# Optimization experiments

Measured on AMD Instinct MI355X. Metric: run time of the kernel, lower is better.

## Reference

```python
import jax, jax.numpy as jnp
import numpy as np

NUM_EMBEDDINGS = 512
EMBEDDING_DIM = 100
COMMITMENT_COST = 0.25


def setup_inputs() -> dict:
    key = jax.random.key(0)
    k1, k2 = jax.random.split(key)
    inputs = jax.random.normal(k1, (64, 64, 64, EMBEDDING_DIM), dtype=jnp.float32)
    # nn.Embedding weight init: uniform(-1/num_embeddings, 1/num_embeddings)
    lim = 1.0 / NUM_EMBEDDINGS
    embedding = jax.random.uniform(k2, (NUM_EMBEDDINGS, EMBEDDING_DIM),
                                   dtype=jnp.float32, minval=-lim, maxval=lim)
    return {"inputs": inputs, "embedding": embedding}


def reference(inputs, embedding):
    d = inputs.shape[-1]
    flat = inputs.reshape(-1, d)                                  # [N, d]
    # squared L2 distances to each codebook entry: [N, K]
    distances = (jnp.sum(flat ** 2, axis=1, keepdims=True)
                 + jnp.sum(embedding ** 2, axis=1)
                 - 2.0 * flat @ embedding.T)
    encoding_indices = jnp.argmin(distances, axis=1)              # [N]
    quantized = embedding[encoding_indices].reshape(inputs.shape)
    commitment_loss = COMMITMENT_COST * jnp.mean(
        (jax.lax.stop_gradient(quantized) - inputs) ** 2)
    quantization_loss = jnp.mean(
        (quantized - jax.lax.stop_gradient(inputs)) ** 2)
    # straight-through estimator
    quantized_st = inputs + jax.lax.stop_gradient(quantized - inputs)
    return quantized_st, quantization_loss, commitment_loss
```

## Files before the change

### kernel.cpp

```cpp
#include <hip/hip_runtime.h>
#include <hip/hip_bf16.h>
#include <cfloat>


#define N_ROWS (64 * 64 * 64)
#define D 100
#define KCODES 512
#define CB_OFF 4096
#define E2_OFF 16

typedef __attribute__((ext_vector_type(8))) short short8;
typedef __attribute__((ext_vector_type(4))) float f32x4;

__device__ __forceinline__ unsigned short f2bf(float f) {
    union { float f; unsigned u; } v; v.f = f;
    unsigned r = v.u + 0x7FFF + ((v.u >> 16) & 1);
    return (unsigned short)(r >> 16);
}
__device__ __forceinline__ unsigned pk2(float a, float b) {
    union { __hip_bfloat162 h; unsigned u; } c;
    c.h = __float22bfloat162_rn(make_float2(a, b));
    return c.u;
}
__device__ __forceinline__ short8 pack8(const float4& a, const float4& b) {
    union { unsigned u[4]; short8 v; } r;
    r.u[0] = pk2(a.x, a.y); r.u[1] = pk2(a.z, a.w);
    r.u[2] = pk2(b.x, b.y); r.u[3] = pk2(b.z, b.w);
    return r.v;
}
__device__ __forceinline__ unsigned f2u(float f) {
    union { float f; unsigned u; } v; v.f = f; return v.u;
}
__device__ __forceinline__ float u2f(unsigned u) {
    union { unsigned u; float f; } v; v.u = u; return v.f;
}

__global__ __launch_bounds__(64) void vq_init(const float* __restrict__ emb,
                                              float* __restrict__ ws) {
    const int code = blockIdx.x, l = threadIdx.x;
    const float* e = emb + code * D;
    if (code == 0 && l == 0) ws[0] = 0.0f;
    float a = e[l];
    float b = (l < D - 64) ? e[64 + l] : 0.0f;
    float p = fmaf(a, a, b * b);
#pragma unroll
    for (int off = 32; off; off >>= 1) p += __shfl_xor(p, off);
    if (l == 0) ws[E2_OFF + code] = p;

    if (l < 16) {
        const int s = l >> 2, q = l & 3;
        short8 v;
#pragma unroll
        for (int j = 0; j < 8; ++j) {
            int k = s * 32 + q * 8 + j;
            v[j] = (k < D) ? (short)f2bf(e[k]) : (short)0;
        }
        if (l == 12) v[4] = (short)f2bf(-0.5f * p);
        const int chunk = code >> 5, ci = code & 31;
        const int tt = ci >> 4, lr = ci & 15;
        unsigned short* cb = (unsigned short*)((char*)ws + CB_OFF);
        *(short8*)(cb + chunk * 4096 + ((s * 2 + tt) * 64 + q * 16 + lr) * 8) = v;
    }
}

__global__ __launch_bounds__(256, 2) void vq_main(const float* __restrict__ x,
                                                  const float* __restrict__ emb,
                                                  float* __restrict__ ws,
                                                  float* __restrict__ out) {
    __shared__ uint4  bbuf[2][1024];
    __shared__ int    widx[256];
    __shared__ float  wsum[4];

    const int tid = threadIdx.x, wave = tid >> 6, lane = tid & 63;
    const int quad = lane >> 4, lr = lane & 15;
    const int lrc = 15 - lr;
    const long brow = (long)blockIdx.x * 256;
    const long wrow = brow + wave * 64;

    float4 av[4][7];
#pragma unroll
    for (int m = 0; m < 4; ++m) {
        const float* xr = x + (wrow + m * 16 + lr) * D + quad * 8;
        av[m][0] = *(const float4*)(xr);
        av[m][1] = *(const float4*)(xr + 4);
        av[m][2] = *(const float4*)(xr + 32);
        av[m][3] = *(const float4*)(xr + 36);
        av[m][4] = *(const float4*)(xr + 64);
        av[m][5] = *(const float4*)(xr + 68);
        av[m][6] = *(const float4*)(x + (wrow + m * 16 + lr) * D + 96);
    }

    const uint4* __restrict__ cbg = (const uint4*)((const char*)ws + CB_OFF);
    uint4 st0 = cbg[wave * 128 + lane];
    uint4 st1 = cbg[wave * 128 + 64 + lane];
    uint4 st2 = cbg[512 + wave * 128 + lane];
    uint4 st3 = cbg[512 + wave * 128 + 64 + lane];

    short8 A[4][4];
    float  xnorm[4];
    const float4 one0 = make_float4(quad == 0 ? 1.f : 0.f, 0.f, 0.f, 0.f);
#pragma unroll
    for (int m = 0; m < 4; ++m) {
        float4 z = av[m][6];
        if (quad != 0) z = make_float4(0.f, 0.f, 0.f, 0.f);
        float nrm = 0.f;
#pragma unroll
        for (int i = 0; i < 6; ++i) {
            float4 f = av[m][i];
            nrm = fmaf(f.x, f.x, nrm); nrm = fmaf(f.y, f.y, nrm);
            nrm = fmaf(f.z, f.z, nrm); nrm = fmaf(f.w, f.w, nrm);
        }
        nrm = fmaf(z.x, z.x, nrm); nrm = fmaf(z.y, z.y, nrm);
        nrm = fmaf(z.z, z.z, nrm); nrm = fmaf(z.w, z.w, nrm);
        A[m][0] = pack8(av[m][0], av[m][1]);
        A[m][1] = pack8(av[m][2], av[m][3]);
        A[m][2] = pack8(av[m][4], av[m][5]);
        A[m][3] = pack8(z, one0);
        nrm += __shfl_xor(nrm, 16);
        nrm += __shfl_xor(nrm, 32);
        xnorm[m] = nrm;
    }

    bbuf[0][wave * 128 + lane]             = st0;
    bbuf[0][wave * 128 + 64 + lane]        = st1;
    bbuf[0][512 + wave * 128 + lane]       = st2;
    bbuf[0][512 + wave * 128 + 64 + lane]  = st3;
    __syncthreads();

    float runpk[4][4];
#pragma unroll
    for (int m = 0; m < 4; ++m)
#pragma unroll
        for (int r = 0; r < 4; ++r) runpk[m][r] = -FLT_MAX;

#pragma unroll 1
    for (int j = 0; j < 8; ++j) {
        const int p = j & 1;
        uint4 n0, n1, n2, n3;
        if (j < 7) {
            n0 = cbg[(j + 1) * 1024 + wave * 128 + lane];
            n1 = cbg[(j + 1) * 1024 + wave * 128 + 64 + lane];
            n2 = cbg[(j + 1) * 1024 + 512 + wave * 128 + lane];
            n3 = cbg[(j + 1) * 1024 + 512 + wave * 128 + 64 + lane];
        }

#pragma unroll
        for (int cc = 0; cc < 2; ++cc) {
            const int c = j * 2 + cc;
            const short8* __restrict__ bl = (const short8*)&bbuf[p][cc * 512];
            short8 B[2][4];
#pragma unroll
            for (int s = 0; s < 4; ++s) {
                B[0][s] = bl[(s * 2 + 0) * 64 + lane];
                B[1][s] = bl[(s * 2 + 1) * 64 + lane];
            }

            f32x4 acc[4][2];
#pragma unroll
            for (int m = 0; m < 4; ++m) {
                acc[m][0] = (f32x4){0.f, 0.f, 0.f, 0.f};
                acc[m][1] = (f32x4){0.f, 0.f, 0.f, 0.f};
            }
#pragma unroll
            for (int s = 0; s < 4; ++s)
#pragma unroll
                for (int m = 0; m < 4; ++m) {
                    acc[m][0] = __builtin_amdgcn_mfma_f32_16x16x32_bf16(A[m][s], B[0][s], acc[m][0], 0, 0, 0);
                    acc[m][1] = __builtin_amdgcn_mfma_f32_16x16x32_bf16(A[m][s], B[1][s], acc[m][1], 0, 0, 0);
                }

            const int ib0 = (31 - (c * 2 + 0)) * 16 + lrc;
            const int ib1 = (31 - (c * 2 + 1)) * 16 + lrc;
#pragma unroll
            for (int m = 0; m < 4; ++m)
#pragma unroll
                for (int r = 0; r < 4; ++r) {
                    float p0 = u2f((f2u(acc[m][0][r]) & ~511u) | (unsigned)ib0);
                    float p1 = u2f((f2u(acc[m][1][r]) & ~511u) | (unsigned)ib1);
                    runpk[m][r] = fmaxf(runpk[m][r], fmaxf(p0, p1));
                }
        }

        if (j < 7) {
            bbuf[p ^ 1][wave * 128 + lane]            = n0;
            bbuf[p ^ 1][wave * 128 + 64 + lane]       = n1;
            bbuf[p ^ 1][512 + wave * 128 + lane]      = n2;
            bbuf[p ^ 1][512 + wave * 128 + 64 + lane] = n3;
        }
        __syncthreads();
    }

    float lsum = 0.0f;
#pragma unroll
    for (int m = 0; m < 4; ++m)
#pragma unroll
        for (int r = 0; r < 4; ++r) {
            float s = runpk[m][r];
#pragma unroll
            for (int off = 8; off >= 1; off >>= 1)
                s = fmaxf(s, __shfl_xor(s, off));
            if (lr == quad * 4 + r) {
                unsigned u = f2u(s);
                int code = 511 - (int)(u & 511u);
                lsum += fmaf(-2.0f, s, xnorm[m]);
                widx[wave * 64 + m * 16 + quad * 4 + r] = code;
            }
        }
#pragma unroll
    for (int off = 32; off >= 1; off >>= 1) lsum += __shfl_xor(lsum, off);
    if (lane == 0) wsum[wave] = lsum;
    __syncthreads();
    if (tid == 0) atomicAdd(ws, wsum[0] + wsum[1] + wsum[2] + wsum[3]);

    const float4* __restrict__ ef = (const float4*)emb;
    float4* __restrict__ og = (float4*)(out + brow * D);
#pragma unroll
    for (int i = 0; i < 25; i += 5) {
        float4 q[5];
        int    gi[5];
#pragma unroll
        for (int u = 0; u < 5; ++u) {
            int g = (i + u) * 256 + tid;
            int row = g / 25;
            int c4  = g - row * 25;
            gi[u] = g;
            q[u]  = ef[(long)widx[row] * 25 + c4];
        }
#pragma unroll
        for (int u = 0; u < 5; ++u) og[gi[u]] = q[u];
    }
}

__global__ void vq_final(const float* __restrict__ ws, float* __restrict__ out) {
    float mse = ws[0] / (float)((long)N_ROWS * D);
    out[(long)N_ROWS * D]     = mse;
    out[(long)N_ROWS * D + 1] = 0.25f * mse;
}

extern "C" void kernel_launch(void* const* d_in, const int* in_sizes, int n_in,
                              void* d_out, int out_size, void* d_ws, size_t ws_size,
                              hipStream_t stream) {
    const float* x   = (const float*)d_in[0];
    const float* emb = (const float*)d_in[1];
    float* out = (float*)d_out;
    float* ws  = (float*)d_ws;

    vq_init<<<KCODES, 64, 0, stream>>>(emb, ws);
    vq_main<<<N_ROWS / 256, 256, 0, stream>>>(x, emb, ws, out);
    vq_final<<<1, 1, 0, stream>>>(ws, out);
}
```

Measured before the change: 214.6 us.

## Switch distance GEMM from bf16 to fp8 MFMA with scaled codebook

Converts the input rows and codebook to fp8 e4m3 and uses the 16x16x32 fp8 MFMA instead of bf16. The codebook is pre-scaled by 512 so its tiny values fit the fp8 range, and the norm term is folded in with matching scaling. This halves codebook staging traffic and LDS footprint and raises MFMA throughput. The cost is much coarser distances, which risks wrong argmin choices and loss values that no longer match the reference.

Result: no change. 213.4 us (-0.5%).

```diff
diff --git a/kernel.cpp b/kernel.cpp
--- a/kernel.cpp
+++ b/kernel.cpp
@@ -1,5 +1,6 @@
 #include <hip/hip_runtime.h>
 #include <hip/hip_bf16.h>
+#include <hip/hip_fp8.h>
 #include <cfloat>
 
 
@@ -9,31 +10,48 @@
 #define CB_OFF 4096
 #define E2_OFF 16
 
-typedef __attribute__((ext_vector_type(8))) short short8;
 typedef __attribute__((ext_vector_type(4))) float f32x4;
 
-__device__ __forceinline__ unsigned short f2bf(float f) {
-    union { float f; unsigned u; } v; v.f = f;
-    unsigned r = v.u + 0x7FFF + ((v.u >> 16) & 1);
-    return (unsigned short)(r >> 16);
-}
-__device__ __forceinline__ unsigned pk2(float a, float b) {
-    union { __hip_bfloat162 h; unsigned u; } c;
-    c.h = __float22bfloat162_rn(make_float2(a, b));
-    return c.u;
-}
-__device__ __forceinline__ short8 pack8(const float4& a, const float4& b) {
-    union { unsigned u[4]; short8 v; } r;
-    r.u[0] = pk2(a.x, a.y); r.u[1] = pk2(a.z, a.w);
-    r.u[2] = pk2(b.x, b.y); r.u[3] = pk2(b.z, b.w);
-    return r.v;
-}
 __device__ __forceinline__ unsigned f2u(float f) {
     union { float f; unsigned u; } v; v.f = f; return v.u;
 }
 __device__ __forceinline__ float u2f(unsigned u) {
     union { unsigned u; float f; } v; v.u = u; return v.f;
 }
+
+__device__ unsigned char f2fp8_sw(float f) {
+    float a = fabsf(f);
+    unsigned sg = (f < 0.f) ? 0x80u : 0u;
+    if (!(a > 0.f)) return (unsigned char)sg;
+    if (a >= 448.f) return (unsigned char)(sg | 0x7E);
+    int ex; float mant = frexpf(a, &ex);
+    int E = ex + 6;
+    int bits;
+    if (E <= 0) {
+        bits = (int)rintf(a * 512.0f);
+    } else {
+        int m = (int)rintf(mant * 16.0f) - 8;
+        if (m == 8) { E++; m = 0; }
+        bits = (E << 3) | m;
+    }
+    return (unsigned char)(sg | bits);
+}
+
+__device__ __forceinline__ unsigned pk4f8(float a, float b, float c, float d) {
+#if __has_builtin(__builtin_amdgcn_cvt_pk_fp8_f32)
+    int v = __builtin_amdgcn_cvt_pk_fp8_f32(a, b, 0, false);
+    v = __builtin_amdgcn_cvt_pk_fp8_f32(c, d, v, true);
+    return (unsigned)v;
+#else
+    union { __hip_fp8x2_e4m3 h; unsigned short s; } lo, hi;
+    lo.h = __hip_fp8x2_e4m3(float2{a, b});
+    hi.h = __hip_fp8x2_e4m3(float2{c, d});
+    return (unsigned)lo.s | ((unsigned)hi.s << 16);
+#endif
+}
+
+union DW2 { unsigned d[2]; long long l; };
+union U4L { uint4 v; long long l[2]; };
 
 __global__ __launch_bounds__(64) void vq_init(const float* __restrict__ emb,
                                               float* __restrict__ ws) {
@@ -47,19 +65,18 @@
     for (int off = 32; off; off >>= 1) p += __shfl_xor(p, off);
     if (l == 0) ws[E2_OFF + code] = p;
 
-    if (l < 16) {
-        const int s = l >> 2, q = l & 3;
-        short8 v;
-#pragma unroll
-        for (int j = 0; j < 8; ++j) {
-            int k = s * 32 + q * 8 + j;
-            v[j] = (k < D) ? (short)f2bf(e[k]) : (short)0;
-        }
-        if (l == 12) v[4] = (short)f2bf(-0.5f * p);
+    if (l < 8) {
+        const int s2 = l >> 2, q = l & 3;
+        union { unsigned char c[16]; uint4 v; } u;
+#pragma unroll
+        for (int j = 0; j < 16; ++j) {
+            int k = s2 * 64 + (j >> 3) * 32 + q * 8 + (j & 7);
+            float v = (k < D) ? e[k] * 512.0f : (k == D ? -p * 256.0f : 0.0f);
+            u.c[j] = f2fp8_sw(v);
+        }
         const int chunk = code >> 5, ci = code & 31;
         const int tt = ci >> 4, lr = ci & 15;
-        unsigned short* cb = (unsigned short*)((char*)ws + CB_OFF);
-        *(short8*)(cb + chunk * 4096 + ((s * 2 + tt) * 64 + q * 16 + lr) * 8) = v;
+        ((uint4*)((char*)ws + CB_OFF))[chunk * 256 + (tt * 2 + s2) * 64 + q * 16 + lr] = u.v;
     }
 }
 
@@ -67,7 +84,7 @@
                                                   const float* __restrict__ emb,
                                                   float* __restrict__ ws,
                                                   float* __restrict__ out) {
-    __shared__ uint4  bbuf[2][1024];
+    __shared__ uint4  bbuf[2][512];
     __shared__ int    widx[256];
     __shared__ float  wsum[4];
 
@@ -91,14 +108,12 @@
     }
 
     const uint4* __restrict__ cbg = (const uint4*)((const char*)ws + CB_OFF);
-    uint4 st0 = cbg[wave * 128 + lane];
-    uint4 st1 = cbg[wave * 128 + 64 + lane];
-    uint4 st2 = cbg[512 + wave * 128 + lane];
-    uint4 st3 = cbg[512 + wave * 128 + 64 + lane];
-
-    short8 A[4][4];
-    float  xnorm[4];
-    const float4 one0 = make_float4(quad == 0 ? 1.f : 0.f, 0.f, 0.f, 0.f);
+    uint4 st0 = cbg[tid];
+    uint4 st1 = cbg[256 + tid];
+
+    long long A8[4][4];
+    float     xnorm[4];
+    const float one0 = (quad == 0) ? 1.0f : 0.0f;
 #pragma unroll
     for (int m = 0; m < 4; ++m) {
         float4 z = av[m][6];
@@ -112,19 +127,23 @@
         }
         nrm = fmaf(z.x, z.x, nrm); nrm = fmaf(z.y, z.y, nrm);
         nrm = fmaf(z.z, z.z, nrm); nrm = fmaf(z.w, z.w, nrm);
-        A[m][0] = pack8(av[m][0], av[m][1]);
-        A[m][1] = pack8(av[m][2], av[m][3]);
-        A[m][2] = pack8(av[m][4], av[m][5]);
-        A[m][3] = pack8(z, one0);
+        DW2 w;
+#pragma unroll
+        for (int s = 0; s < 3; ++s) {
+            w.d[0] = pk4f8(av[m][2*s].x, av[m][2*s].y, av[m][2*s].z, av[m][2*s].w);
+            w.d[1] = pk4f8(av[m][2*s+1].x, av[m][2*s+1].y, av[m][2*s+1].z, av[m][2*s+1].w);
+            A8[m][s] = w.l;
+        }
+        w.d[0] = pk4f8(z.x, z.y, z.z, z.w);
+        w.d[1] = pk4f8(one0, 0.f, 0.f, 0.f);
+        A8[m][3] = w.l;
         nrm += __shfl_xor(nrm, 16);
         nrm += __shfl_xor(nrm, 32);
         xnorm[m] = nrm;
     }
 
-    bbuf[0][wave * 128 + lane]             = st0;
-    bbuf[0][wave * 128 + 64 + lane]        = st1;
-    bbuf[0][512 + wave * 128 + lane]       = st2;
-    bbuf[0][512 + wave * 128 + 64 + lane]  = st3;
+    bbuf[0][tid]       = st0;
+    bbuf[0][256 + tid] = st1;
     __syncthreads();
 
     float runpk[4][4];
@@ -136,24 +155,23 @@
 #pragma unroll 1
     for (int j = 0; j < 8; ++j) {
         const int p = j & 1;
-        uint4 n0, n1, n2, n3;
+        uint4 n0, n1;
         if (j < 7) {
-            n0 = cbg[(j + 1) * 1024 + wave * 128 + lane];
-            n1 = cbg[(j + 1) * 1024 + wave * 128 + 64 + lane];
-            n2 = cbg[(j + 1) * 1024 + 512 + wave * 128 + lane];
-            n3 = cbg[(j + 1) * 1024 + 512 + wave * 128 + 64 + lane];
+            n0 = cbg[(j + 1) * 512 + tid];
+            n1 = cbg[(j + 1) * 512 + 256 + tid];
         }
 
 #pragma unroll
         for (int cc = 0; cc < 2; ++cc) {
             const int c = j * 2 + cc;
-            const short8* __restrict__ bl = (const short8*)&bbuf[p][cc * 512];
-            short8 B[2][4];
-#pragma unroll
-            for (int s = 0; s < 4; ++s) {
-                B[0][s] = bl[(s * 2 + 0) * 64 + lane];
-                B[1][s] = bl[(s * 2 + 1) * 64 + lane];
-            }
+            const uint4* __restrict__ bl = &bbuf[p][cc * 256];
+            U4L q0, q1, q2, q3;
+            q0.v = bl[lane];
+            q1.v = bl[64 + lane];
+            q2.v = bl[128 + lane];
+            q3.v = bl[192 + lane];
+            long long B0[4] = { q0.l[0], q0.l[1], q1.l[0], q1.l[1] };
+            long long B1[4] = { q2.l[0], q2.l[1], q3.l[0], q3.l[1] };
 
             f32x4 acc[4][2];
 #pragma unroll
@@ -165,8 +183,8 @@
             for (int s = 0; s < 4; ++s)
 #pragma unroll
                 for (int m = 0; m < 4; ++m) {
-                    acc[m][0] = __builtin_amdgcn_mfma_f32_16x16x32_bf16(A[m][s], B[0][s], acc[m][0], 0, 0, 0);
-                    acc[m][1] = __builtin_amdgcn_mfma_f32_16x16x32_bf16(A[m][s], B[1][s], acc[m][1], 0, 0, 0);
+                    acc[m][0] = __builtin_amdgcn_mfma_f32_16x16x32_fp8_fp8(A8[m][s], B0[s], acc[m][0], 0, 0, 0);
+                    acc[m][1] = __builtin_amdgcn_mfma_f32_16x16x32_fp8_fp8(A8[m][s], B1[s], acc[m][1], 0, 0, 0);
                 }
 
             const int ib0 = (31 - (c * 2 + 0)) * 16 + lrc;
@@ -182,10 +200,8 @@
         }
 
         if (j < 7) {
-            bbuf[p ^ 1][wave * 128 + lane]            = n0;
-            bbuf[p ^ 1][wave * 128 + 64 + lane]       = n1;
-            bbuf[p ^ 1][512 + wave * 128 + lane]      = n2;
-            bbuf[p ^ 1][512 + wave * 128 + 64 + lane] = n3;
+            bbuf[p ^ 1][tid]       = n0;
+            bbuf[p ^ 1][256 + tid] = n1;
         }
         __syncthreads();
     }
@@ -202,7 +218,7 @@
             if (lr == quad * 4 + r) {
                 unsigned u = f2u(s);
                 int code = 511 - (int)(u & 511u);
-                lsum += fmaf(-2.0f, s, xnorm[m]);
+                lsum += fmaf(-0.00390625f, s, xnorm[m]);
                 widx[wave * 64 + m * 16 + quad * 4 + r] = code;
             }
         }
```

## Switch distance GEMM to 32x32x16 bf16 MFMA with tighter K packing

Applied to the files above, without the earlier changes.

Replaces the 16x16x32 MFMA tiling with 32x32x16 bf16 MFMAs, repacking the codebook layout and input fragments so that K covers 112 (100 dims plus a bias slot) instead of 128. This cuts wasted MFMA work on zero padding and shrinks the shared codebook buffer, and it changes the argmax reduction to 32-wide shuffles. It raises accumulator register pressure (two 16-float accumulators per chunk) and changes the per-lane row mapping in the reduction.

Result: slower. 220.6 us (+2.8%).

```diff
diff --git a/kernel.cpp b/kernel.cpp
--- a/kernel.cpp
+++ b/kernel.cpp
@@ -10,7 +10,7 @@
 #define E2_OFF 16
 
 typedef __attribute__((ext_vector_type(8))) short short8;
-typedef __attribute__((ext_vector_type(4))) float f32x4;
+typedef __attribute__((ext_vector_type(16))) float f32x16;
 
 __device__ __forceinline__ unsigned short f2bf(float f) {
     union { float f; unsigned u; } v; v.f = f;
@@ -47,19 +47,18 @@
     for (int off = 32; off; off >>= 1) p += __shfl_xor(p, off);
     if (l == 0) ws[E2_OFF + code] = p;
 
-    if (l < 16) {
-        const int s = l >> 2, q = l & 3;
+    if (l < 14) {
+        const int s = l >> 1, hi = l & 1;
         short8 v;
 #pragma unroll
         for (int j = 0; j < 8; ++j) {
-            int k = s * 32 + q * 8 + j;
-            v[j] = (k < D) ? (short)f2bf(e[k]) : (short)0;
-        }
-        if (l == 12) v[4] = (short)f2bf(-0.5f * p);
-        const int chunk = code >> 5, ci = code & 31;
-        const int tt = ci >> 4, lr = ci & 15;
-        unsigned short* cb = (unsigned short*)((char*)ws + CB_OFF);
-        *(short8*)(cb + chunk * 4096 + ((s * 2 + tt) * 64 + q * 16 + lr) * 8) = v;
+            int k = s * 16 + hi * 8 + j;
+            float val = (k < D) ? e[k] : (k == D ? -0.5f * p : 0.0f);
+            v[j] = (short)f2bf(val);
+        }
+        const int chunk = code >> 5, col = code & 31;
+        short8* cb = (short8*)((char*)ws + CB_OFF);
+        cb[chunk * 448 + (s * 2 + hi) * 32 + col] = v;
     }
 }
 
@@ -67,143 +66,133 @@
                                                   const float* __restrict__ emb,
                                                   float* __restrict__ ws,
                                                   float* __restrict__ out) {
-    __shared__ uint4  bbuf[2][1024];
+    __shared__ uint4  bbuf[2][896];
     __shared__ int    widx[256];
     __shared__ float  wsum[4];
 
     const int tid = threadIdx.x, wave = tid >> 6, lane = tid & 63;
-    const int quad = lane >> 4, lr = lane & 15;
-    const int lrc = 15 - lr;
+    const int hi = lane >> 5, col = lane & 31;
     const long brow = (long)blockIdx.x * 256;
     const long wrow = brow + wave * 64;
 
-    float4 av[4][7];
-#pragma unroll
-    for (int m = 0; m < 4; ++m) {
-        const float* xr = x + (wrow + m * 16 + lr) * D + quad * 8;
-        av[m][0] = *(const float4*)(xr);
-        av[m][1] = *(const float4*)(xr + 4);
-        av[m][2] = *(const float4*)(xr + 32);
-        av[m][3] = *(const float4*)(xr + 36);
-        av[m][4] = *(const float4*)(xr + 64);
-        av[m][5] = *(const float4*)(xr + 68);
-        av[m][6] = *(const float4*)(x + (wrow + m * 16 + lr) * D + 96);
+    float4 av[2][13];
+#pragma unroll
+    for (int t = 0; t < 2; ++t) {
+        const float* xr = x + (wrow + t * 32 + col) * D + hi * 8;
+#pragma unroll
+        for (int s = 0; s < 6; ++s) {
+            av[t][2 * s]     = *(const float4*)(xr + s * 16);
+            av[t][2 * s + 1] = *(const float4*)(xr + s * 16 + 4);
+        }
+        av[t][12] = *(const float4*)(x + (wrow + t * 32 + col) * D + 96);
     }
 
     const uint4* __restrict__ cbg = (const uint4*)((const char*)ws + CB_OFF);
-    uint4 st0 = cbg[wave * 128 + lane];
-    uint4 st1 = cbg[wave * 128 + 64 + lane];
-    uint4 st2 = cbg[512 + wave * 128 + lane];
-    uint4 st3 = cbg[512 + wave * 128 + 64 + lane];
-
-    short8 A[4][4];
-    float  xnorm[4];
-    const float4 one0 = make_float4(quad == 0 ? 1.f : 0.f, 0.f, 0.f, 0.f);
-#pragma unroll
-    for (int m = 0; m < 4; ++m) {
-        float4 z = av[m][6];
-        if (quad != 0) z = make_float4(0.f, 0.f, 0.f, 0.f);
+    uint4 st0 = cbg[tid];
+    uint4 st1 = cbg[256 + tid];
+    uint4 st2 = cbg[512 + tid];
+    uint4 st3;
+    if (tid < 128) st3 = cbg[768 + tid];
+
+    short8 A8[2][7];
+    float  xnorm[2];
+#pragma unroll
+    for (int t = 0; t < 2; ++t) {
+        float4 z = av[t][12];
+        if (hi != 0) z = make_float4(0.f, 0.f, 0.f, 0.f);
         float nrm = 0.f;
 #pragma unroll
-        for (int i = 0; i < 6; ++i) {
-            float4 f = av[m][i];
+        for (int i = 0; i < 12; ++i) {
+            float4 f = av[t][i];
             nrm = fmaf(f.x, f.x, nrm); nrm = fmaf(f.y, f.y, nrm);
             nrm = fmaf(f.z, f.z, nrm); nrm = fmaf(f.w, f.w, nrm);
         }
         nrm = fmaf(z.x, z.x, nrm); nrm = fmaf(z.y, z.y, nrm);
         nrm = fmaf(z.z, z.z, nrm); nrm = fmaf(z.w, z.w, nrm);
-        A[m][0] = pack8(av[m][0], av[m][1]);
-        A[m][1] = pack8(av[m][2], av[m][3]);
-        A[m][2] = pack8(av[m][4], av[m][5]);
-        A[m][3] = pack8(z, one0);
-        nrm += __shfl_xor(nrm, 16);
+#pragma unroll
+        for (int s = 0; s < 6; ++s) A8[t][s] = pack8(av[t][2 * s], av[t][2 * s + 1]);
+        A8[t][6] = pack8(z, make_float4(hi == 0 ? 1.f : 0.f, 0.f, 0.f, 0.f));
         nrm += __shfl_xor(nrm, 32);
-        xnorm[m] = nrm;
-    }
-
-    bbuf[0][wave * 128 + lane]             = st0;
-    bbuf[0][wave * 128 + 64 + lane]        = st1;
-    bbuf[0][512 + wave * 128 + lane]       = st2;
-    bbuf[0][512 + wave * 128 + 64 + lane]  = st3;
+        xnorm[t] = nrm;
+    }
+
+    bbuf[0][tid]       = st0;
+    bbuf[0][256 + tid] = st1;
+    bbuf[0][512 + tid] = st2;
+    if (tid < 128) bbuf[0][768 + tid] = st3;
     __syncthreads();
 
-    float runpk[4][4];
-#pragma unroll
-    for (int m = 0; m < 4; ++m)
-#pragma unroll
-        for (int r = 0; r < 4; ++r) runpk[m][r] = -FLT_MAX;
+    float run[2][16];
+#pragma unroll
+    for (int t = 0; t < 2; ++t)
+#pragma unroll
+        for (int r = 0; r < 16; ++r) run[t][r] = -FLT_MAX;
+
+    const int ibase = 31 - col;
 
 #pragma unroll 1
     for (int j = 0; j < 8; ++j) {
         const int p = j & 1;
         uint4 n0, n1, n2, n3;
         if (j < 7) {
-            n0 = cbg[(j + 1) * 1024 + wave * 128 + lane];
-            n1 = cbg[(j + 1) * 1024 + wave * 128 + 64 + lane];
-            n2 = cbg[(j + 1) * 1024 + 512 + wave * 128 + lane];
-            n3 = cbg[(j + 1) * 1024 + 512 + wave * 128 + 64 + lane];
-        }
-
+            const int gb = (j + 1) * 896;
+            n0 = cbg[gb + tid];
+            n1 = cbg[gb + 256 + tid];
+            n2 = cbg[gb + 512 + tid];
+            if (tid < 128) n3 = cbg[gb + 768 + tid];
+        }
+
+        f32x16 acc[2][2];
 #pragma unroll
         for (int cc = 0; cc < 2; ++cc) {
-            const int c = j * 2 + cc;
-            const short8* __restrict__ bl = (const short8*)&bbuf[p][cc * 512];
-            short8 B[2][4];
-#pragma unroll
-            for (int s = 0; s < 4; ++s) {
-                B[0][s] = bl[(s * 2 + 0) * 64 + lane];
-                B[1][s] = bl[(s * 2 + 1) * 64 + lane];
+            const short8* __restrict__ bl8 = (const short8*)&bbuf[p][cc * 448];
+            short8 B[7];
+#pragma unroll
+            for (int s = 0; s < 7; ++s) B[s] = bl8[(s * 2 + hi) * 32 + col];
+
+            acc[cc][0] = (f32x16)(0.f);
+            acc[cc][1] = (f32x16)(0.f);
+#pragma unroll
+            for (int s = 0; s < 7; ++s)
+#pragma unroll
+                for (int t = 0; t < 2; ++t)
+                    acc[cc][t] = __builtin_amdgcn_mfma_f32_32x32x16_bf16(A8[t][s], B[s], acc[cc][t], 0, 0, 0);
+        }
+
+        const int ib0 = (15 - 2 * j) * 32 + ibase;
+        const int ib1 = ib0 - 32;
+#pragma unroll
+        for (int t = 0; t < 2; ++t)
+#pragma unroll
+            for (int r = 0; r < 16; ++r) {
+                float p0 = u2f((f2u(acc[0][t][r]) & ~511u) | (unsigned)ib0);
+                float p1 = u2f((f2u(acc[1][t][r]) & ~511u) | (unsigned)ib1);
+                run[t][r] = fmaxf(run[t][r], fmaxf(p0, p1));
             }
 
-            f32x4 acc[4][2];
-#pragma unroll
-            for (int m = 0; m < 4; ++m) {
-                acc[m][0] = (f32x4){0.f, 0.f, 0.f, 0.f};
-                acc[m][1] = (f32x4){0.f, 0.f, 0.f, 0.f};
-            }
-#pragma unroll
-            for (int s = 0; s < 4; ++s)
-#pragma unroll
-                for (int m = 0; m < 4; ++m) {
-                    acc[m][0] = __builtin_amdgcn_mfma_f32_16x16x32_bf16(A[m][s], B[0][s], acc[m][0], 0, 0, 0);
-                    acc[m][1] = __builtin_amdgcn_mfma_f32_16x16x32_bf16(A[m][s], B[1][s], acc[m][1], 0, 0, 0);
-                }
-
-            const int ib0 = (31 - (c * 2 + 0)) * 16 + lrc;
-            const int ib1 = (31 - (c * 2 + 1)) * 16 + lrc;
-#pragma unroll
-            for (int m = 0; m < 4; ++m)
-#pragma unroll
-                for (int r = 0; r < 4; ++r) {
-                    float p0 = u2f((f2u(acc[m][0][r]) & ~511u) | (unsigned)ib0);
-                    float p1 = u2f((f2u(acc[m][1][r]) & ~511u) | (unsigned)ib1);
-                    runpk[m][r] = fmaxf(runpk[m][r], fmaxf(p0, p1));
-                }
-        }
-
         if (j < 7) {
-            bbuf[p ^ 1][wave * 128 + lane]            = n0;
-            bbuf[p ^ 1][wave * 128 + 64 + lane]       = n1;
-            bbuf[p ^ 1][512 + wave * 128 + lane]      = n2;
-            bbuf[p ^ 1][512 + wave * 128 + 64 + lane] = n3;
+            bbuf[p ^ 1][tid]       = n0;
+            bbuf[p ^ 1][256 + tid] = n1;
+            bbuf[p ^ 1][512 + tid] = n2;
+            if (tid < 128) bbuf[p ^ 1][768 + tid] = n3;
         }
         __syncthreads();
     }
 
     float lsum = 0.0f;
 #pragma unroll
-    for (int m = 0; m < 4; ++m)
-#pragma unroll
-        for (int r = 0; r < 4; ++r) {
-            float s = runpk[m][r];
-#pragma unroll
-            for (int off = 8; off >= 1; off >>= 1)
+    for (int t = 0; t < 2; ++t)
+#pragma unroll
+        for (int r = 0; r < 16; ++r) {
+            float s = run[t][r];
+#pragma unroll
+            for (int off = 16; off >= 1; off >>= 1)
                 s = fmaxf(s, __shfl_xor(s, off));
-            if (lr == quad * 4 + r) {
+            const int rowl = (r & 3) + 8 * (r >> 2) + 4 * hi;
+            if (col == rowl) {
                 unsigned u = f2u(s);
-                int code = 511 - (int)(u & 511u);
-                lsum += fmaf(-2.0f, s, xnorm[m]);
-                widx[wave * 64 + m * 16 + quad * 4 + r] = code;
+                widx[wave * 64 + t * 32 + rowl] = 511 - (int)(u & 511u);
+                lsum += fmaf(-2.0f, s, xnorm[t]);
             }
         }
 #pragma unroll
```

## Give each wave a private codebook buffer to remove block barriers

Applied to the files above, without the earlier changes.

Each wave now loads the whole 32-code codebook chunk itself into its own double-buffered LDS region, so the per-iteration __syncthreads is dropped. Before, the four waves cooperatively staged a shared buffer and synchronized every step. This removes barrier stalls and lets waves drift independently. The cost is four times the global/L2 codebook traffic and LDS writes, LDS use grows from 32KB to 64KB per block (risking occupancy at 2 blocks/CU), and more registers are spent on prefetch (8 uint4 instead of 4).

Result: slower. 314.8 us (+46.7%).

```diff
diff --git a/kernel.cpp b/kernel.cpp
--- a/kernel.cpp
+++ b/kernel.cpp
@@ -67,7 +67,7 @@
                                                   const float* __restrict__ emb,
                                                   float* __restrict__ ws,
                                                   float* __restrict__ out) {
-    __shared__ uint4  bbuf[2][1024];
+    __shared__ uint4  pbuf[2][4][512];
     __shared__ int    widx[256];
     __shared__ float  wsum[4];
 
@@ -91,10 +91,9 @@
     }
 
     const uint4* __restrict__ cbg = (const uint4*)((const char*)ws + CB_OFF);
-    uint4 st0 = cbg[wave * 128 + lane];
-    uint4 st1 = cbg[wave * 128 + 64 + lane];
-    uint4 st2 = cbg[512 + wave * 128 + lane];
-    uint4 st3 = cbg[512 + wave * 128 + 64 + lane];
+    uint4 st[8];
+#pragma unroll
+    for (int k = 0; k < 8; ++k) st[k] = cbg[k * 64 + lane];
 
     short8 A[4][4];
     float  xnorm[4];
@@ -121,11 +120,8 @@
         xnorm[m] = nrm;
     }
 
-    bbuf[0][wave * 128 + lane]             = st0;
-    bbuf[0][wave * 128 + 64 + lane]        = st1;
-    bbuf[0][512 + wave * 128 + lane]       = st2;
-    bbuf[0][512 + wave * 128 + 64 + lane]  = st3;
-    __syncthreads();
+#pragma unroll
+    for (int k = 0; k < 8; ++k) pbuf[0][wave][k * 64 + lane] = st[k];
 
     float runpk[4][4];
 #pragma unroll
@@ -134,60 +130,50 @@
         for (int r = 0; r < 4; ++r) runpk[m][r] = -FLT_MAX;
 
 #pragma unroll 1
-    for (int j = 0; j < 8; ++j) {
-        const int p = j & 1;
-        uint4 n0, n1, n2, n3;
-        if (j < 7) {
-            n0 = cbg[(j + 1) * 1024 + wave * 128 + lane];
-            n1 = cbg[(j + 1) * 1024 + wave * 128 + 64 + lane];
-            n2 = cbg[(j + 1) * 1024 + 512 + wave * 128 + lane];
-            n3 = cbg[(j + 1) * 1024 + 512 + wave * 128 + 64 + lane];
-        }
-
-#pragma unroll
-        for (int cc = 0; cc < 2; ++cc) {
-            const int c = j * 2 + cc;
-            const short8* __restrict__ bl = (const short8*)&bbuf[p][cc * 512];
-            short8 B[2][4];
-#pragma unroll
-            for (int s = 0; s < 4; ++s) {
-                B[0][s] = bl[(s * 2 + 0) * 64 + lane];
-                B[1][s] = bl[(s * 2 + 1) * 64 + lane];
+    for (int c = 0; c < 16; ++c) {
+        const int p = c & 1;
+        if (c < 15) {
+#pragma unroll
+            for (int k = 0; k < 8; ++k) st[k] = cbg[(c + 1) * 512 + k * 64 + lane];
+        }
+
+        const short8* __restrict__ bl = (const short8*)&pbuf[p][wave][0];
+        short8 B[2][4];
+#pragma unroll
+        for (int s = 0; s < 4; ++s) {
+            B[0][s] = bl[(s * 2 + 0) * 64 + lane];
+            B[1][s] = bl[(s * 2 + 1) * 64 + lane];
+        }
+
+        f32x4 acc[4][2];
+#pragma unroll
+        for (int m = 0; m < 4; ++m) {
+            acc[m][0] = (f32x4){0.f, 0.f, 0.f, 0.f};
+            acc[m][1] = (f32x4){0.f, 0.f, 0.f, 0.f};
+        }
+#pragma unroll
+        for (int s = 0; s < 4; ++s)
+#pragma unroll
+            for (int m = 0; m < 4; ++m) {
+                acc[m][0] = __builtin_amdgcn_mfma_f32_16x16x32_bf16(A[m][s], B[0][s], acc[m][0], 0, 0, 0);
+                acc[m][1] = __builtin_amdgcn_mfma_f32_16x16x32_bf16(A[m][s], B[1][s], acc[m][1], 0, 0, 0);
             }
 
-            f32x4 acc[4][2];
-#pragma unroll
-            for (int m = 0; m < 4; ++m) {
-                acc[m][0] = (f32x4){0.f, 0.f, 0.f, 0.f};
-                acc[m][1] = (f32x4){0.f, 0.f, 0.f, 0.f};
+        const int ib0 = (31 - (c * 2 + 0)) * 16 + lrc;
+        const int ib1 = (31 - (c * 2 + 1)) * 16 + lrc;
+#pragma unroll
+        for (int m = 0; m < 4; ++m)
+#pragma unroll
+            for (int r = 0; r < 4; ++r) {
+                float p0 = u2f((f2u(acc[m][0][r]) & ~511u) | (unsigned)ib0);
+                float p1 = u2f((f2u(acc[m][1][r]) & ~511u) | (unsigned)ib1);
+                runpk[m][r] = fmaxf(runpk[m][r], fmaxf(p0, p1));
             }
-#pragma unroll
-            for (int s = 0; s < 4; ++s)
-#pragma unroll
-                for (int m = 0; m < 4; ++m) {
-                    acc[m][0] = __builtin_amdgcn_mfma_f32_16x16x32_bf16(A[m][s], B[0][s], acc[m][0], 0, 0, 0);
-                    acc[m][1] = __builtin_amdgcn_mfma_f32_16x16x32_bf16(A[m][s], B[1][s], acc[m][1], 0, 0, 0);
-                }
-
-            const int ib0 = (31 - (c * 2 + 0)) * 16 + lrc;
-            const int ib1 = (31 - (c * 2 + 1)) * 16 + lrc;
-#pragma unroll
-            for (int m = 0; m < 4; ++m)
-#pragma unroll
-                for (int r = 0; r < 4; ++r) {
-                    float p0 = u2f((f2u(acc[m][0][r]) & ~511u) | (unsigned)ib0);
-                    float p1 = u2f((f2u(acc[m][1][r]) & ~511u) | (unsigned)ib1);
-                    runpk[m][r] = fmaxf(runpk[m][r], fmaxf(p0, p1));
-                }
-        }
-
-        if (j < 7) {
-            bbuf[p ^ 1][wave * 128 + lane]            = n0;
-            bbuf[p ^ 1][wave * 128 + 64 + lane]       = n1;
-            bbuf[p ^ 1][512 + wave * 128 + lane]      = n2;
-            bbuf[p ^ 1][512 + wave * 128 + 64 + lane] = n3;
-        }
-        __syncthreads();
+
+        if (c < 15) {
+#pragma unroll
+            for (int k = 0; k < 8; ++k) pbuf[p ^ 1][wave][k * 64 + lane] = st[k];
+        }
     }
 
     float lsum = 0.0f;
```
